# Performance work log

Measured on AMD Instinct MI355X. Metric: run time of the kernel, lower is better.

## Reference

```python
import jax, jax.numpy as jnp
import numpy as np

B, F, E, H = 4096, 26, 64, 1000000
D = F * E  # 1664

def setup_inputs() -> dict:
    key = jax.random.key(0)
    ks = jax.random.split(key, 12)
    s = 0.02  # init scale
    return {
        "ids": jax.random.randint(ks[0], (B, F), 0, H),
        "emb": jax.random.normal(ks[1], (H, E), jnp.float32) * s,
        "cross_w": jax.random.normal(ks[2], (3, D), jnp.float32) * s,
        "cross_b": jnp.zeros((3, D), jnp.float32),
        "w1": jax.random.normal(ks[3], (D, 1024), jnp.float32) * s,
        "b1": jnp.zeros((1024,), jnp.float32),
        "w2": jax.random.normal(ks[4], (1024, 512), jnp.float32) * s,
        "b2": jnp.zeros((512,), jnp.float32),
        "w3": jax.random.normal(ks[5], (512, 256), jnp.float32) * s,
        "b3": jnp.zeros((256,), jnp.float32),
        "out_w": jax.random.normal(ks[6], (D + 256, 1), jnp.float32) * s,
        "out_b": jnp.zeros((), jnp.float32),
    }

def reference(ids, emb, cross_w, cross_b, w1, b1, w2, b2, w3, b3, out_w, out_b):
    # Embedding lookup + field-wise concat -> x0: [B, D]
    x0 = emb[ids].reshape(ids.shape[0], -1)
    # Cross net. Original materializes [B,D,D] outer product x0 * x^T then
    # giving the same math with O(B*D) memory.
    x = x0
    for i in range(cross_w.shape[0]):
        s = x @ cross_w[i]                 # [B] per-example scalar
        x = x0 * s[:, None] + cross_b[i] + x
    # Deep tower on x0
    h = jax.nn.relu(x0 @ w1 + b1)
    h = jax.nn.relu(h @ w2 + b2)
    h = jax.nn.relu(h @ w3 + b3)
    # Output head
    logit = jnp.concatenate([x, h], axis=1) @ out_w + out_b  # [B, 1]
    return jax.nn.sigmoid(logit)
```

## Files before the change

### kernel.cpp

```cpp
#include <hip/hip_runtime.h>
#include <hip/hip_bf16.h>

#define B_  4096
#define F_  26
#define E_  64
#define D_  1664
#define N1_ 1024
#define N2_ 512
#define N3_ 256

typedef __attribute__((ext_vector_type(8))) __bf16 bf16x8;
typedef __attribute__((ext_vector_type(4))) float  f32x4;

__device__ __forceinline__ unsigned short f2b(float x) {
    __hip_bfloat16 h = __float2bfloat16(x);
    return __builtin_bit_cast(unsigned short, h);
}
__device__ __forceinline__ float b2f(unsigned short u) {
    return __uint_as_float(((unsigned)u) << 16);
}

__device__ __forceinline__ void async_load16(const void* g, void* l) {
    __builtin_amdgcn_global_load_lds(
        (const __attribute__((address_space(1))) void*)g,
        (__attribute__((address_space(3))) void*)l,
        16, 0, 0);
}

__device__ __forceinline__ f32x4 mfma16(bf16x8 a, bf16x8 b, f32x4 c) {
    return __builtin_amdgcn_mfma_f32_16x16x32_bf16(a, b, c, 0, 0, 0);
}

__global__ __launch_bounds__(256) void gather_cross_kernel(
        const int* __restrict__ ids, const float* __restrict__ emb,
        const float* __restrict__ cw, const float* __restrict__ cb,
        const float* __restrict__ out_w,
        unsigned short* __restrict__ x0out, float* __restrict__ partial)
{
    __shared__ int   sid[F_];
    __shared__ float red[4];
    const int b = blockIdx.x;
    const int t = threadIdx.x;
    const int lane = t & 63, w = t >> 6;
    constexpr int C4 = D_ / 4;

    if (t < F_) sid[t] = ids[b * F_ + t];
    __syncthreads();

    const float4* emb4 = (const float4*)emb;
    const float4* cw4  = (const float4*)cw;
    const float4* cb4  = (const float4*)cb;
    const float4* ow4  = (const float4*)out_w;

    float4 x0v[2], xv[2];
    #pragma unroll
    for (int j = 0; j < 2; j++) {
        const int c = t + j * 256;
        float4 v = make_float4(0.f, 0.f, 0.f, 0.f);
        if (c < C4) {
            const int f = c >> 4;
            v = emb4[(size_t)sid[f] * 16 + (c & 15)];
            ushort4 o;
            o.x = f2b(v.x); o.y = f2b(v.y); o.z = f2b(v.z); o.w = f2b(v.w);
            ((ushort4*)x0out)[(size_t)b * C4 + c] = o;
        }
        x0v[j] = v; xv[j] = v;
    }
    for (int i = 0; i < 3; i++) {
        float s = 0.f;
        #pragma unroll
        for (int j = 0; j < 2; j++) {
            const int c = t + j * 256;
            if (c < C4) {
                const float4 wv = cw4[i * C4 + c];
                s += xv[j].x * wv.x + xv[j].y * wv.y + xv[j].z * wv.z + xv[j].w * wv.w;
            }
        }
        #pragma unroll
        for (int off = 32; off > 0; off >>= 1) s += __shfl_down(s, off, 64);
        __syncthreads();
        if (lane == 0) red[w] = s;
        __syncthreads();
        const float st = red[0] + red[1] + red[2] + red[3];
        #pragma unroll
        for (int j = 0; j < 2; j++) {
            const int c = t + j * 256;
            if (c < C4) {
                const float4 bv = cb4[i * C4 + c];
                xv[j].x = x0v[j].x * st + bv.x + xv[j].x;
                xv[j].y = x0v[j].y * st + bv.y + xv[j].y;
                xv[j].z = x0v[j].z * st + bv.z + xv[j].z;
                xv[j].w = x0v[j].w * st + bv.w + xv[j].w;
            }
        }
    }
    float s = 0.f;
    #pragma unroll
    for (int j = 0; j < 2; j++) {
        const int c = t + j * 256;
        if (c < C4) {
            const float4 wv = ow4[c];
            s += xv[j].x * wv.x + xv[j].y * wv.y + xv[j].z * wv.z + xv[j].w * wv.w;
        }
    }
    #pragma unroll
    for (int off = 32; off > 0; off >>= 1) s += __shfl_down(s, off, 64);
    __syncthreads();
    if (lane == 0) red[w] = s;
    __syncthreads();
    if (t == 0) partial[b] = red[0] + red[1] + red[2] + red[3];
}

__global__ __launch_bounds__(256) void transpose_all_kernel(
        const float* __restrict__ w1, const float* __restrict__ w2,
        const float* __restrict__ w3,
        unsigned short* __restrict__ o1, unsigned short* __restrict__ o2,
        unsigned short* __restrict__ o3)
{
    __shared__ float tile[32][33];
    const int bid = blockIdx.x;
    const float* in; unsigned short* out; int K, N, lg, t0;
    if (bid < 1664)      { in = w1; out = o1; K = D_;  N = N1_; lg = 5; t0 = 0;    }
    else if (bid < 2176) { in = w2; out = o2; K = N1_; N = N2_; lg = 4; t0 = 1664; }
    else                 { in = w3; out = o3; K = N2_; N = N3_; lg = 3; t0 = 2176; }
    const int tl = bid - t0;
    const int n0 = (tl & ((1 << lg) - 1)) * 32;
    const int k0 = (tl >> lg) * 32;
    const int tc = threadIdx.x & 31, tr = threadIdx.x >> 5;
    #pragma unroll
    for (int p = 0; p < 4; p++)
        tile[tr + p * 8][tc] = in[(size_t)(k0 + tr + p * 8) * N + n0 + tc];
    __syncthreads();
    #pragma unroll
    for (int p = 0; p < 4; p++) {
        const int n = tr + p * 8;
        out[(size_t)(n0 + n) * K + k0 + tc] = f2b(tile[tc][n]);
    }
}

template<int BM, int BN, int BKC>
__global__ __launch_bounds__(256, 4) void gemm_bias_relu(
        const unsigned short* __restrict__ A,
        const unsigned short* __restrict__ Bt,
        const float* __restrict__ bias,
        unsigned short* __restrict__ C,
        int M, int N, int K)
{
    constexpr int KU = BKC / 32;
    constexpr int WM = BM / 2, WN = BN / 2;
    constexpr int TI = WM / 16, TJ = WN / 16;
    constexpr int nA = BM / 16, nB = BN / 16, nAB = nA + nB;
    constexpr int TOTC = KU * nAB;

    __shared__ unsigned short sA[KU * BM * 32];
    __shared__ unsigned short sB[KU * BN * 32];

    const int t    = threadIdx.x;
    const int lane = t & 63;
    const int w    = t >> 6;

    const int i    = blockIdx.y * gridDim.x + blockIdx.x;
    const int xcd  = i & 7;
    const int s    = i >> 3;
    const int ypg  = gridDim.y >> 3;
    const int ty   = xcd * ypg + s / gridDim.x;
    const int tx   = s - (s / gridDim.x) * gridDim.x;
    const int m0   = ty * BM;
    const int n0   = tx * BN;
    const int wm   = (w >> 1) * WM;
    const int wn   = (w & 1) * WN;

    const int srow = lane >> 2;
    const int scol = (lane & 3) * 8;

    f32x4 acc[TI][TJ] = {};

    for (int k0 = 0; k0 < K; k0 += BKC) {
        #pragma unroll
        for (int c0 = 0; c0 < TOTC; c0 += 4) {
            const int c = c0 + w;
            const int u = c / nAB;
            const int r = c - u * nAB;
            if (r < nA) {
                const unsigned short* g =
                    A + (size_t)(m0 + r * 16 + srow) * K + k0 + u * 32 + scol;
                async_load16(g, &sA[u * BM * 32 + r * 512]);
            } else {
                const int rb = r - nA;
                const unsigned short* g =
                    Bt + (size_t)(n0 + rb * 16 + srow) * K + k0 + u * 32 + scol;
                async_load16(g, &sB[u * BN * 32 + rb * 512]);
            }
        }
        __syncthreads();

        #pragma unroll
        for (int u = 0; u < KU; u++) {
            bf16x8 af[TI], bf[TJ];
            #pragma unroll
            for (int ii = 0; ii < TI; ii++)
                af[ii] = *(const bf16x8*)
                    &sA[u * BM * 32 + (wm + ii * 16 + (lane & 15)) * 32 + (lane >> 4) * 8];
            #pragma unroll
            for (int j = 0; j < TJ; j++)
                bf[j] = *(const bf16x8*)
                    &sB[u * BN * 32 + (wn + j * 16 + (lane & 15)) * 32 + (lane >> 4) * 8];
            #pragma unroll
            for (int ii = 0; ii < TI; ii++)
                #pragma unroll
                for (int j = 0; j < TJ; j++)
                    acc[ii][j] = mfma16(af[ii], bf[j], acc[ii][j]);
        }
        __syncthreads();
    }

    #pragma unroll
    for (int ii = 0; ii < TI; ii++) {
        const int r0 = m0 + wm + ii * 16 + (lane >> 4) * 4;
        #pragma unroll
        for (int j = 0; j < TJ; j++) {
            const int col = n0 + wn + j * 16 + (lane & 15);
            const float bv = bias[col];
            #pragma unroll
            for (int r = 0; r < 4; r++) {
                float v = acc[ii][j][r] + bv;
                v = fmaxf(v, 0.f);
                C[(size_t)(r0 + r) * N + col] = f2b(v);
            }
        }
    }
}

__global__ __launch_bounds__(256) void head_kernel(
        const float* __restrict__ partial, const unsigned short* __restrict__ h3,
        const float* __restrict__ out_w, const float* __restrict__ out_b,
        float* __restrict__ out)
{
    const int gw   = (blockIdx.x * 256 + threadIdx.x) >> 6;
    const int lane = threadIdx.x & 63;
    if (gw >= B_) return;
    float s = 0.f;
    #pragma unroll
    for (int q = 0; q < 4; q++) {
        const int j = lane + q * 64;
        s += b2f(h3[(size_t)gw * N3_ + j]) * out_w[D_ + j];
    }
    #pragma unroll
    for (int off = 32; off > 0; off >>= 1) s += __shfl_down(s, off, 64);
    if (lane == 0) {
        const float logit = partial[gw] + s + out_b[0];
        out[gw] = 1.f / (1.f + expf(-logit));
    }
}

extern "C" void kernel_launch(void* const* d_in, const int* in_sizes, int n_in,
                              void* d_out, int out_size, void* d_ws, size_t ws_size,
                              hipStream_t stream)
{
    (void)in_sizes; (void)n_in; (void)out_size; (void)ws_size;
    const int*   ids     = (const int*)  d_in[0];
    const float* emb     = (const float*)d_in[1];
    const float* cross_w = (const float*)d_in[2];
    const float* cross_b = (const float*)d_in[3];
    const float* w1      = (const float*)d_in[4];
    const float* b1      = (const float*)d_in[5];
    const float* w2      = (const float*)d_in[6];
    const float* b2      = (const float*)d_in[7];
    const float* w3      = (const float*)d_in[8];
    const float* b3      = (const float*)d_in[9];
    const float* out_w   = (const float*)d_in[10];
    const float* out_b   = (const float*)d_in[11];
    float* out = (float*)d_out;

    char* p = (char*)d_ws;
    auto alloc = [&](size_t bytes) {
        char* r = p; p += (bytes + 255) & ~(size_t)255; return r;
    };
    unsigned short* x0b = (unsigned short*)alloc((size_t)B_ * D_ * 2);
    unsigned short* w1t = (unsigned short*)alloc((size_t)D_ * N1_ * 2);
    unsigned short* w2t = (unsigned short*)alloc((size_t)N1_ * N2_ * 2);
    unsigned short* w3t = (unsigned short*)alloc((size_t)N2_ * N3_ * 2);
    unsigned short* h1  = (unsigned short*)alloc((size_t)B_ * N1_ * 2);
    unsigned short* h2  = (unsigned short*)alloc((size_t)B_ * N2_ * 2);
    unsigned short* h3  = (unsigned short*)alloc((size_t)B_ * N3_ * 2);
    float* partial      = (float*)alloc((size_t)B_ * 4);

    gather_cross_kernel<<<B_, 256, 0, stream>>>(
        ids, emb, cross_w, cross_b, out_w, x0b, partial);
    transpose_all_kernel<<<2304, 256, 0, stream>>>(w1, w2, w3, w1t, w2t, w3t);

    gemm_bias_relu<64, 64, 128><<<dim3(N1_ / 64, B_ / 64), 256, 0, stream>>>(
        x0b, w1t, b1, h1, B_, N1_, D_);
    gemm_bias_relu<64, 32, 128><<<dim3(N2_ / 32, B_ / 64), 256, 0, stream>>>(
        h1, w2t, b2, h2, B_, N2_, N1_);
    gemm_bias_relu<32, 32, 128><<<dim3(N3_ / 32, B_ / 32), 256, 0, stream>>>(
        h2, w3t, b3, h3, B_, N3_, N2_);

    head_kernel<<<B_ / 4, 256, 0, stream>>>(partial, h3, out_w, out_b, out);
}
```

Measured before the change: 379.6 us.

## Fuse gather/cross and weight transpose into one launch, retile GEMMs

Merges the embedding gather + cross-net kernel and the weight transpose kernel into a single launch, with extra blocks doing the transpose, which removes one kernel launch and lets both run concurrently. The cross kernel now preloads all cross weights and biases into registers up front and uses double-buffered reduction slots, dropping one barrier per iteration. The three GEMMs switch to taller M tiles with a smaller K chunk. Register pressure and the different tile shapes may change occupancy.

```diff
diff --git a/kernel.cpp b/kernel.cpp
--- a/kernel.cpp
+++ b/kernel.cpp
@@ -31,111 +31,123 @@
     return __builtin_amdgcn_mfma_f32_16x16x32_bf16(a, b, c, 0, 0, 0);
 }
 
-__global__ __launch_bounds__(256) void gather_cross_kernel(
+__global__ __launch_bounds__(256) void gather_cross_transpose_kernel(
         const int* __restrict__ ids, const float* __restrict__ emb,
         const float* __restrict__ cw, const float* __restrict__ cb,
         const float* __restrict__ out_w,
-        unsigned short* __restrict__ x0out, float* __restrict__ partial)
-{
-    __shared__ int   sid[F_];
-    __shared__ float red[4];
-    const int b = blockIdx.x;
-    const int t = threadIdx.x;
-    const int lane = t & 63, w = t >> 6;
-    constexpr int C4 = D_ / 4;
-
-    if (t < F_) sid[t] = ids[b * F_ + t];
-    __syncthreads();
-
-    const float4* emb4 = (const float4*)emb;
-    const float4* cw4  = (const float4*)cw;
-    const float4* cb4  = (const float4*)cb;
-    const float4* ow4  = (const float4*)out_w;
-
-    float4 x0v[2], xv[2];
-    #pragma unroll
-    for (int j = 0; j < 2; j++) {
-        const int c = t + j * 256;
-        float4 v = make_float4(0.f, 0.f, 0.f, 0.f);
-        if (c < C4) {
-            const int f = c >> 4;
-            v = emb4[(size_t)sid[f] * 16 + (c & 15)];
-            ushort4 o;
-            o.x = f2b(v.x); o.y = f2b(v.y); o.z = f2b(v.z); o.w = f2b(v.w);
-            ((ushort4*)x0out)[(size_t)b * C4 + c] = o;
-        }
-        x0v[j] = v; xv[j] = v;
-    }
-    for (int i = 0; i < 3; i++) {
-        float s = 0.f;
-        #pragma unroll
-        for (int j = 0; j < 2; j++) {
-            const int c = t + j * 256;
-            if (c < C4) {
-                const float4 wv = cw4[i * C4 + c];
-                s += xv[j].x * wv.x + xv[j].y * wv.y + xv[j].z * wv.z + xv[j].w * wv.w;
-            }
-        }
-        #pragma unroll
-        for (int off = 32; off > 0; off >>= 1) s += __shfl_down(s, off, 64);
-        __syncthreads();
-        if (lane == 0) red[w] = s;
-        __syncthreads();
-        const float st = red[0] + red[1] + red[2] + red[3];
-        #pragma unroll
-        for (int j = 0; j < 2; j++) {
-            const int c = t + j * 256;
-            if (c < C4) {
-                const float4 bv = cb4[i * C4 + c];
-                xv[j].x = x0v[j].x * st + bv.x + xv[j].x;
-                xv[j].y = x0v[j].y * st + bv.y + xv[j].y;
-                xv[j].z = x0v[j].z * st + bv.z + xv[j].z;
-                xv[j].w = x0v[j].w * st + bv.w + xv[j].w;
-            }
-        }
-    }
-    float s = 0.f;
-    #pragma unroll
-    for (int j = 0; j < 2; j++) {
-        const int c = t + j * 256;
-        if (c < C4) {
-            const float4 wv = ow4[c];
-            s += xv[j].x * wv.x + xv[j].y * wv.y + xv[j].z * wv.z + xv[j].w * wv.w;
-        }
-    }
-    #pragma unroll
-    for (int off = 32; off > 0; off >>= 1) s += __shfl_down(s, off, 64);
-    __syncthreads();
-    if (lane == 0) red[w] = s;
-    __syncthreads();
-    if (t == 0) partial[b] = red[0] + red[1] + red[2] + red[3];
-}
-
-__global__ __launch_bounds__(256) void transpose_all_kernel(
+        unsigned short* __restrict__ x0out, float* __restrict__ partial,
         const float* __restrict__ w1, const float* __restrict__ w2,
         const float* __restrict__ w3,
         unsigned short* __restrict__ o1, unsigned short* __restrict__ o2,
         unsigned short* __restrict__ o3)
 {
+    __shared__ int   sid[F_];
+    __shared__ float red[2][4];
     __shared__ float tile[32][33];
-    const int bid = blockIdx.x;
-    const float* in; unsigned short* out; int K, N, lg, t0;
-    if (bid < 1664)      { in = w1; out = o1; K = D_;  N = N1_; lg = 5; t0 = 0;    }
-    else if (bid < 2176) { in = w2; out = o2; K = N1_; N = N2_; lg = 4; t0 = 1664; }
-    else                 { in = w3; out = o3; K = N2_; N = N3_; lg = 3; t0 = 2176; }
-    const int tl = bid - t0;
-    const int n0 = (tl & ((1 << lg) - 1)) * 32;
-    const int k0 = (tl >> lg) * 32;
-    const int tc = threadIdx.x & 31, tr = threadIdx.x >> 5;
-    #pragma unroll
-    for (int p = 0; p < 4; p++)
-        tile[tr + p * 8][tc] = in[(size_t)(k0 + tr + p * 8) * N + n0 + tc];
+
+    if (blockIdx.x >= B_) {
+        const int bid = blockIdx.x - B_;
+        const float* in; unsigned short* out; int K, N, lg, t0;
+        if (bid < 1664)      { in = w1; out = o1; K = D_;  N = N1_; lg = 5; t0 = 0;    }
+        else if (bid < 2176) { in = w2; out = o2; K = N1_; N = N2_; lg = 4; t0 = 1664; }
+        else                 { in = w3; out = o3; K = N2_; N = N3_; lg = 3; t0 = 2176; }
+        const int tl = bid - t0;
+        const int n0 = (tl & ((1 << lg) - 1)) * 32;
+        const int k0 = (tl >> lg) * 32;
+        const int tc = threadIdx.x & 31, tr = threadIdx.x >> 5;
+        #pragma unroll
+        for (int p = 0; p < 4; p++)
+            tile[tr + p * 8][tc] = in[(size_t)(k0 + tr + p * 8) * N + n0 + tc];
+        __syncthreads();
+        #pragma unroll
+        for (int p = 0; p < 4; p++) {
+            const int n = tr + p * 8;
+            out[(size_t)(n0 + n) * K + k0 + tc] = f2b(tile[tc][n]);
+        }
+        return;
+    }
+
+    const int b = blockIdx.x;
+    const int t = threadIdx.x;
+    const int lane = t & 63, w = t >> 6;
+    constexpr int C4 = D_ / 4;
+
+    if (t < F_) sid[t] = ids[b * F_ + t];
     __syncthreads();
-    #pragma unroll
-    for (int p = 0; p < 4; p++) {
-        const int n = tr + p * 8;
-        out[(size_t)(n0 + n) * K + k0 + tc] = f2b(tile[tc][n]);
-    }
+
+    const float4* emb4 = (const float4*)emb;
+    const float4* cw4  = (const float4*)cw;
+    const float4* cb4  = (const float4*)cb;
+    const float4* ow4  = (const float4*)out_w;
+
+    const float4 z4 = make_float4(0.f, 0.f, 0.f, 0.f);
+    float4 x0v[2], xv[2];
+    float4 cwv[3][2], cbv[3][2], owv[2];
+
+    #pragma unroll
+    for (int j = 0; j < 2; j++) {
+        const int c = t + j * 256;
+        float4 v = z4;
+        if (c < C4) {
+            const int f = c >> 4;
+            v = emb4[(size_t)sid[f] * 16 + (c & 15)];
+        }
+        x0v[j] = v; xv[j] = v;
+    }
+    #pragma unroll
+    for (int i = 0; i < 3; i++)
+        #pragma unroll
+        for (int j = 0; j < 2; j++) {
+            const int c = t + j * 256;
+            cwv[i][j] = (c < C4) ? cw4[i * C4 + c] : z4;
+            cbv[i][j] = (c < C4) ? cb4[i * C4 + c] : z4;
+        }
+    #pragma unroll
+    for (int j = 0; j < 2; j++) {
+        const int c = t + j * 256;
+        owv[j] = (c < C4) ? ow4[c] : z4;
+    }
+    #pragma unroll
+    for (int j = 0; j < 2; j++) {
+        const int c = t + j * 256;
+        if (c < C4) {
+            ushort4 o;
+            o.x = f2b(x0v[j].x); o.y = f2b(x0v[j].y);
+            o.z = f2b(x0v[j].z); o.w = f2b(x0v[j].w);
+            ((ushort4*)x0out)[(size_t)b * C4 + c] = o;
+        }
+    }
+
+    #pragma unroll
+    for (int i = 0; i < 3; i++) {
+        float s = 0.f;
+        #pragma unroll
+        for (int j = 0; j < 2; j++)
+            s += xv[j].x * cwv[i][j].x + xv[j].y * cwv[i][j].y
+               + xv[j].z * cwv[i][j].z + xv[j].w * cwv[i][j].w;
+        #pragma unroll
+        for (int off = 32; off > 0; off >>= 1) s += __shfl_down(s, off, 64);
+        if (lane == 0) red[i & 1][w] = s;
+        __syncthreads();
+        const float st = red[i & 1][0] + red[i & 1][1] + red[i & 1][2] + red[i & 1][3];
+        #pragma unroll
+        for (int j = 0; j < 2; j++) {
+            xv[j].x = x0v[j].x * st + cbv[i][j].x + xv[j].x;
+            xv[j].y = x0v[j].y * st + cbv[i][j].y + xv[j].y;
+            xv[j].z = x0v[j].z * st + cbv[i][j].z + xv[j].z;
+            xv[j].w = x0v[j].w * st + cbv[i][j].w + xv[j].w;
+        }
+    }
+    float s = 0.f;
+    #pragma unroll
+    for (int j = 0; j < 2; j++)
+        s += xv[j].x * owv[j].x + xv[j].y * owv[j].y
+           + xv[j].z * owv[j].z + xv[j].w * owv[j].w;
+    #pragma unroll
+    for (int off = 32; off > 0; off >>= 1) s += __shfl_down(s, off, 64);
+    if (lane == 0) red[1][w] = s;
+    __syncthreads();
+    if (t == 0) partial[b] = red[1][0] + red[1][1] + red[1][2] + red[1][3];
 }
 
 template<int BM, int BN, int BKC>
@@ -151,6 +163,7 @@
     constexpr int TI = WM / 16, TJ = WN / 16;
     constexpr int nA = BM / 16, nB = BN / 16, nAB = nA + nB;
     constexpr int TOTC = KU * nAB;
+    static_assert(TOTC % 4 == 0, "chunk loop assumes 4-wave coverage");
 
     __shared__ unsigned short sA[KU * BM * 32];
     __shared__ unsigned short sB[KU * BN * 32];
@@ -285,15 +298,15 @@
     unsigned short* h3  = (unsigned short*)alloc((size_t)B_ * N3_ * 2);
     float* partial      = (float*)alloc((size_t)B_ * 4);
 
-    gather_cross_kernel<<<B_, 256, 0, stream>>>(
-        ids, emb, cross_w, cross_b, out_w, x0b, partial);
-    transpose_all_kernel<<<2304, 256, 0, stream>>>(w1, w2, w3, w1t, w2t, w3t);
-
-    gemm_bias_relu<64, 64, 128><<<dim3(N1_ / 64, B_ / 64), 256, 0, stream>>>(
+    gather_cross_transpose_kernel<<<B_ + 2304, 256, 0, stream>>>(
+        ids, emb, cross_w, cross_b, out_w, x0b, partial,
+        w1, w2, w3, w1t, w2t, w3t);
+
+    gemm_bias_relu<128, 64, 64><<<dim3(N1_ / 64, B_ / 128), 256, 0, stream>>>(
         x0b, w1t, b1, h1, B_, N1_, D_);
-    gemm_bias_relu<64, 32, 128><<<dim3(N2_ / 32, B_ / 64), 256, 0, stream>>>(
+    gemm_bias_relu<128, 32, 64><<<dim3(N2_ / 32, B_ / 128), 256, 0, stream>>>(
         h1, w2t, b2, h2, B_, N2_, N1_);
-    gemm_bias_relu<32, 32, 128><<<dim3(N3_ / 32, B_ / 32), 256, 0, stream>>>(
+    gemm_bias_relu<64, 32, 64><<<dim3(N3_ / 32, B_ / 64), 256, 0, stream>>>(
         h2, w3t, b3, h3, B_, N3_, N2_);
 
     head_kernel<<<B_ / 4, 256, 0, stream>>>(partial, h3, out_w, out_b, out);
```

New measurement: 403.5 us. 1.06x slower.
